# Optimization experiments

Hardware: AMD Instinct MI355X
Metric: run time of the kernel (lower is better)

The kernel has to match this reference:

```python
import jax, jax.numpy as jnp
import numpy as np

NUM_EMBEDDINGS = 8192
EMBEDDING_DIM = 512
COMMITMENT_COST = 0.25


def setup_inputs() -> dict:
    key = jax.random.key(0)
    kx, ke = jax.random.split(key)
    x = jax.random.normal(kx, (32, 512, 512), dtype=jnp.float32)
    # codebook ~ uniform init as in nn.Embedding default-ish; scale is arbitrary for a reference
    codebook = jax.random.normal(ke, (NUM_EMBEDDINGS, EMBEDDING_DIM), dtype=jnp.float32)
    return {"x": x, "codebook": codebook}


def reference(x, codebook):
    # x: [B, T, D], codebook: [K, D]
    input_shape = x.shape
    flat = x.reshape(-1, EMBEDDING_DIM)                     # [N, D]
    x2 = jnp.sum(flat * flat, axis=1, keepdims=True)        # [N, 1]
    e2 = jnp.sum(codebook * codebook, axis=1)               # [K]
    dists = x2 + e2 - 2.0 * jnp.matmul(flat, codebook.T)    # [N, K]
    encoding_indices = jnp.argmin(dists, axis=1)            # [N] int
    min_distances = jnp.min(dists, axis=1)                  # [N]
    quantized = codebook[encoding_indices].reshape(input_shape)  # [B, T, D]
    # straight-through estimator
    quantized_st = x + jax.lax.stop_gradient(quantized - x)
    # losses (sum reduction, matching F.mse_loss(..., reduction='sum'))
    loss_vq = jnp.sum((quantized - jax.lax.stop_gradient(x)) ** 2)
    loss_commit = jnp.sum((x - jax.lax.stop_gradient(quantized)) ** 2)
    # use_ema = False -> loss includes codebook term
    loss = loss_commit * COMMITMENT_COST + loss_vq
    encoding_indices = encoding_indices.reshape(input_shape[:-1])
    min_distances = min_distances.reshape(input_shape[:-1])
    return quantized_st, loss, encoding_indices, min_distances, loss_commit
```

## Files before the change

### kernel.cpp

```cpp
#include <hip/hip_runtime.h>
#include <hip/hip_bf16.h>
#include <math.h>

#define NUM_EMB 8192
#define DIM 512
#define NROWS 16384
#define NPART 4096

typedef unsigned short ushort;
typedef unsigned long long ull;
typedef __attribute__((ext_vector_type(8))) short short8;
typedef __attribute__((ext_vector_type(4))) float floatx4;

__device__ __forceinline__ ushort f2bf(float f) {
    unsigned u = __float_as_uint(f);
    unsigned r = (u + 0x7fffu + ((u >> 16) & 1u)) >> 16;
    return (ushort)r;
}
__device__ __forceinline__ float bf2f(ushort h) {
    return __uint_as_float(((unsigned)h) << 16);
}
__device__ __forceinline__ unsigned fmap(float f) {
    unsigned u = __float_as_uint(f);
    return (u & 0x80000000u) ? ~u : (u | 0x80000000u);
}
__device__ __forceinline__ float funmap(unsigned m) {
    return __uint_as_float((m & 0x80000000u) ? (m ^ 0x80000000u) : ~m);
}
__device__ __forceinline__ void gld16(const void* g, void* l) {
    __builtin_amdgcn_global_load_lds(
        (const __attribute__((address_space(1))) void*)g,
        (__attribute__((address_space(3))) void*)l, 16, 0, 0);
}

__global__ __launch_bounds__(256) void split_rss_k(const float* __restrict__ src,
    ushort* __restrict__ hi, ushort* __restrict__ lo, float* __restrict__ ss,
    ull* __restrict__ packed, int nrows)
{
    int gid  = blockIdx.x * blockDim.x + threadIdx.x;
    int row  = gid >> 6;
    int lane = threadIdx.x & 63;
    if (row >= nrows) return;
    const float4* r = (const float4*)(src + (size_t)row * DIM);
    ushort4* h4 = (ushort4*)(hi + (size_t)row * DIM);
    ushort4* l4 = (ushort4*)(lo + (size_t)row * DIM);
    float s = 0.f;
#pragma unroll
    for (int i = lane; i < DIM / 4; i += 64) {
        float4 v = r[i];
        s += v.x * v.x + v.y * v.y + v.z * v.z + v.w * v.w;
        ushort4 h, l;
        h.x = f2bf(v.x); l.x = f2bf(v.x - bf2f(h.x));
        h.y = f2bf(v.y); l.y = f2bf(v.y - bf2f(h.y));
        h.z = f2bf(v.z); l.z = f2bf(v.z - bf2f(h.z));
        h.w = f2bf(v.w); l.w = f2bf(v.w - bf2f(h.w));
        h4[i] = h; l4[i] = l;
    }
#pragma unroll
    for (int off = 32; off > 0; off >>= 1) s += __shfl_down(s, off, 64);
    if (lane == 0) {
        ss[row] = s;
        if (packed) packed[row] = ~0ull;
    }
}

__global__ __launch_bounds__(512, 2) void dist_mfma_k(
    const ushort* __restrict__ xh, const ushort* __restrict__ xl,
    const ushort* __restrict__ ch, const ushort* __restrict__ cl,
    const float* __restrict__ e2, ull* __restrict__ packed)
{
    __shared__ ushort Ah[2][256 * 32];
    __shared__ ushort Al[2][256 * 32];
    __shared__ ushort Bh[2][256 * 32];
    __shared__ ushort Bl[2][256 * 32];

    const int tid  = threadIdx.x;
    const int lane = tid & 63;
    const int w    = tid >> 6;
    const int wm   = w >> 2, wn = w & 3;
    const int row0 = blockIdx.x * 256;
    const int col0 = blockIdx.y * 256;

    floatx4 acc[8][4];
#pragma unroll
    for (int m = 0; m < 8; ++m)
#pragma unroll
        for (int n = 0; n < 4; ++n) acc[m][n] = (floatx4){0.f, 0.f, 0.f, 0.f};

    const int u = tid & 255, b = tid >> 8;
    const int p = u & 3;
    const int r_h0 = b * 128 + (u >> 2);
    const int r_h1 = r_h0 + 64;
    const int seg0 = (p ^ ((r_h0 >> 1) & 3)) * 8;
    const int seg1 = (p ^ ((r_h1 >> 1) & 3)) * 8;
    const int lo_h0 = (r_h0 * 4 + p) * 8;
    const int lo_h1 = (r_h1 * 4 + p) * 8;
    const int gA0 = (row0 + r_h0) * DIM + seg0;
    const int gA1 = (row0 + r_h1) * DIM + seg1;
    const int gB0 = (col0 + r_h0) * DIM + seg0;
    const int gB1 = (col0 + r_h1) * DIM + seg1;

    const int fr = (lane & 15) * 32 + (((lane >> 4) ^ ((lane >> 1) & 3)) * 8);

    short8 ah[4], al[4], bh[4], bl[4];

#define ISSUE_A(B_, h_, dk_) do { \
    if (h_) { gld16(&xh[gA1 + (dk_)], &Ah[B_][lo_h1]); gld16(&xl[gA1 + (dk_)], &Al[B_][lo_h1]); } \
    else    { gld16(&xh[gA0 + (dk_)], &Ah[B_][lo_h0]); gld16(&xl[gA0 + (dk_)], &Al[B_][lo_h0]); } } while (0)
#define ISSUE_B(B_, h_, dk_) do { \
    if (h_) { gld16(&ch[gB1 + (dk_)], &Bh[B_][lo_h1]); gld16(&cl[gB1 + (dk_)], &Bl[B_][lo_h1]); } \
    else    { gld16(&ch[gB0 + (dk_)], &Bh[B_][lo_h0]); gld16(&cl[gB0 + (dk_)], &Bl[B_][lo_h0]); } } while (0)
#define LOAD_A(B_, mh_) do { \
    _Pragma("unroll") for (int m = 0; m < 4; ++m) { \
        const int o = (wm * 128 + (mh_) * 64 + m * 16) * 32 + fr; \
        ah[m] = *(const short8*)&Ah[B_][o]; \
        al[m] = *(const short8*)&Al[B_][o]; } } while (0)
#define LOAD_B(B_, nh_) do { \
    _Pragma("unroll") for (int n = 0; n < 2; ++n) { \
        const int o = (wn * 64 + (nh_) * 32 + n * 16) * 32 + fr; \
        bh[(nh_) * 2 + n] = *(const short8*)&Bh[B_][o]; \
        bl[(nh_) * 2 + n] = *(const short8*)&Bl[B_][o]; } } while (0)
#define DO_MFMA(mh_, nh_) do { \
    __builtin_amdgcn_s_setprio(1); \
    _Pragma("unroll") for (int m = 0; m < 4; ++m) \
    _Pragma("unroll") for (int n = 0; n < 2; ++n) { \
        acc[(mh_) * 4 + m][(nh_) * 2 + n] = __builtin_amdgcn_mfma_f32_16x16x32_bf16(ah[m], bh[(nh_) * 2 + n], acc[(mh_) * 4 + m][(nh_) * 2 + n], 0, 0, 0); \
        acc[(mh_) * 4 + m][(nh_) * 2 + n] = __builtin_amdgcn_mfma_f32_16x16x32_bf16(ah[m], bl[(nh_) * 2 + n], acc[(mh_) * 4 + m][(nh_) * 2 + n], 0, 0, 0); \
        acc[(mh_) * 4 + m][(nh_) * 2 + n] = __builtin_amdgcn_mfma_f32_16x16x32_bf16(al[m], bh[(nh_) * 2 + n], acc[(mh_) * 4 + m][(nh_) * 2 + n], 0, 0, 0); \
    } \
    __builtin_amdgcn_s_setprio(0); } while (0)

    ISSUE_A(0, 0, 0);
    ISSUE_B(0, 0, 0);
    ISSUE_B(0, 1, 0);
    ISSUE_A(0, 1, 0);
    asm volatile("s_waitcnt vmcnt(0)" ::: "memory");
    __builtin_amdgcn_s_barrier();
    __builtin_amdgcn_sched_barrier(0);

#pragma unroll 1
    for (int t = 0; t < 16; ++t) {
        const int B = t & 1, Bn = B ^ 1;
        const int dkn = (t + 1) * 32;
        const bool pf = (t < 15);

        LOAD_A(B, 0);
        LOAD_B(B, 0);
        if (pf) ISSUE_A(Bn, 0, dkn);
        DO_MFMA(0, 0);
        if (pf) { asm volatile("s_waitcnt vmcnt(4)" ::: "memory"); }
        else    { asm volatile("s_waitcnt vmcnt(2)" ::: "memory"); }
        __builtin_amdgcn_s_barrier();
        __builtin_amdgcn_sched_barrier(0);

        LOAD_B(B, 1);
        if (pf) ISSUE_B(Bn, 0, dkn);
        DO_MFMA(0, 1);
        if (pf) { asm volatile("s_waitcnt vmcnt(4)" ::: "memory"); }
        else    { asm volatile("s_waitcnt vmcnt(0)" ::: "memory"); }
        __builtin_amdgcn_s_barrier();
        __builtin_amdgcn_sched_barrier(0);

        LOAD_A(B, 1);
        if (pf) ISSUE_B(Bn, 1, dkn);
        DO_MFMA(1, 1);
        __builtin_amdgcn_s_barrier();
        __builtin_amdgcn_sched_barrier(0);

        if (pf) ISSUE_A(Bn, 1, dkn);
        DO_MFMA(1, 0);
        if (pf) { asm volatile("s_waitcnt vmcnt(4)" ::: "memory"); }
        __builtin_amdgcn_s_barrier();
        __builtin_amdgcn_sched_barrier(0);
    }

#undef ISSUE_A
#undef ISSUE_B
#undef LOAD_A
#undef LOAD_B
#undef DO_MFMA

    float e2v[4];
    int   cidx[4];
#pragma unroll
    for (int n = 0; n < 4; ++n) {
        cidx[n] = col0 + wn * 64 + n * 16 + (lane & 15);
        e2v[n]  = e2[cidx[n]];
    }
#pragma unroll
    for (int m = 0; m < 8; ++m) {
#pragma unroll
        for (int r = 0; r < 4; ++r) {
            float bv = INFINITY; int bi = 0x7fffffff;
#pragma unroll
            for (int n = 0; n < 4; ++n) {
                float v = e2v[n] - 2.f * acc[m][n][r];
                if (v < bv) { bv = v; bi = cidx[n]; }
            }
#pragma unroll
            for (int mk = 1; mk < 16; mk <<= 1) {
                float ov = __shfl_xor(bv, mk, 64);
                int   oi = __shfl_xor(bi, mk, 64);
                if (ov < bv || (ov == bv && oi < bi)) { bv = ov; bi = oi; }
            }
            if ((lane & 15) == 0) {
                int grow = row0 + wm * 128 + m * 16 + (lane >> 4) * 4 + r;
                ull pack = ((ull)fmap(bv) << 32) | (unsigned)bi;
                atomicMin(&packed[grow], pack);
            }
        }
    }
}

__global__ __launch_bounds__(256) void gather_loss_k(const float* __restrict__ x,
    const float* __restrict__ cb, const ull* __restrict__ packed,
    const float* __restrict__ x2, float* __restrict__ outq,
    float* __restrict__ out_idx, float* __restrict__ out_mind,
    float* __restrict__ partials)
{
    __shared__ float ps[4];
    int gid  = blockIdx.x * blockDim.x + threadIdx.x;
    int row  = gid >> 6;
    int lane = threadIdx.x & 63;
    int w    = threadIdx.x >> 6;
    float s = 0.f;
    if (row < NROWS) {
        ull p = packed[row];
        int k = (int)(p & 0xffffffffull);
        if (lane == 0) {
            out_idx[row]  = (float)k;
            out_mind[row] = x2[row] + funmap((unsigned)(p >> 32));
        }
        const float4* q  = (const float4*)(cb + (size_t)k * DIM);
        const float4* xr = (const float4*)(x + (size_t)row * DIM);
        float4* o = (float4*)(outq + (size_t)row * DIM);
#pragma unroll
        for (int i = lane; i < DIM / 4; i += 64) {
            float4 qv = q[i], xv = xr[i];
            o[i] = qv;
            float dx = xv.x - qv.x, dy = xv.y - qv.y;
            float dz = xv.z - qv.z, dw = xv.w - qv.w;
            s += dx * dx + dy * dy + dz * dz + dw * dw;
        }
    }
#pragma unroll
    for (int off = 32; off > 0; off >>= 1) s += __shfl_down(s, off, 64);
    if (lane == 0) ps[w] = s;
    __syncthreads();
    if (threadIdx.x == 0) partials[blockIdx.x] = ps[0] + ps[1] + ps[2] + ps[3];
}

__global__ __launch_bounds__(256) void finalize_k(const float* __restrict__ partials,
    float* __restrict__ out_loss, float* __restrict__ out_commit)
{
    __shared__ float ps[4];
    int t = threadIdx.x, lane = t & 63, w = t >> 6;
    float s = 0.f;
#pragma unroll
    for (int i = 0; i < NPART / 256; ++i) s += partials[t + 256 * i];
#pragma unroll
    for (int off = 32; off > 0; off >>= 1) s += __shfl_down(s, off, 64);
    if (lane == 0) ps[w] = s;
    __syncthreads();
    if (t == 0) {
        float tot = ps[0] + ps[1] + ps[2] + ps[3];
        *out_loss   = 0.25f * tot + tot;
        *out_commit = tot;
    }
}

#define BM 64
#define BN 64
#define BK 32
#define KSPLIT 4
#define KPER (NUM_EMB / KSPLIT)
#define NCT (KPER / BN)

__global__ __launch_bounds__(256) void rowsumsq_k(const float* __restrict__ a,
                                                  float* __restrict__ out, int nrows)
{
    int gid  = blockIdx.x * blockDim.x + threadIdx.x;
    int row  = gid >> 6;
    int lane = threadIdx.x & 63;
    if (row >= nrows) return;
    const float4* r = (const float4*)(a + (size_t)row * DIM);
    float s = 0.f;
#pragma unroll
    for (int i = lane; i < DIM / 4; i += 64) {
        float4 v = r[i];
        s += v.x * v.x + v.y * v.y + v.z * v.z + v.w * v.w;
    }
#pragma unroll
    for (int off = 32; off > 0; off >>= 1) s += __shfl_down(s, off, 64);
    if (lane == 0) out[row] = s;
}

__global__ __launch_bounds__(256) void dist_argmin_old_k(const float* __restrict__ x,
    const float* __restrict__ cb, const float* __restrict__ e2,
    float* __restrict__ part_m, int* __restrict__ part_i)
{
    __shared__ __align__(16) float As[BK][BM + 4];
    __shared__ __align__(16) float Bs[BK][BN + 4];
    __shared__ float redv[BM][16];
    __shared__ int   redi[BM][16];

    const int row0 = blockIdx.x * BM;
    const int ks   = blockIdx.y;
    const int cbeg = ks * KPER;
    const int t    = threadIdx.x;
    const int tx   = t & 15;
    const int ty   = t >> 4;
    const int ld_d = t & 31;
    const int ld_r = t >> 5;

    float minm[4]; int mini[4];
#pragma unroll
    for (int i = 0; i < 4; ++i) { minm[i] = INFINITY; mini[i] = 0; }

    for (int ct = 0; ct < NCT; ++ct) {
        const int c0 = cbeg + ct * BN;
        float acc[4][4];
#pragma unroll
        for (int i = 0; i < 4; ++i)
#pragma unroll
            for (int j = 0; j < 4; ++j) acc[i][j] = 0.f;
        for (int dc = 0; dc < DIM; dc += BK) {
#pragma unroll
            for (int rr = 0; rr < BM; rr += 8)
                As[ld_d][ld_r + rr] = x[(size_t)(row0 + ld_r + rr) * DIM + dc + ld_d];
#pragma unroll
            for (int rr = 0; rr < BN; rr += 8)
                Bs[ld_d][ld_r + rr] = cb[(size_t)(c0 + ld_r + rr) * DIM + dc + ld_d];
            __syncthreads();
#pragma unroll
            for (int d = 0; d < BK; ++d) {
                float4 av = *(const float4*)&As[d][4 * ty];
                float4 bv = *(const float4*)&Bs[d][4 * tx];
                acc[0][0] += av.x * bv.x; acc[0][1] += av.x * bv.y;
                acc[0][2] += av.x * bv.z; acc[0][3] += av.x * bv.w;
                acc[1][0] += av.y * bv.x; acc[1][1] += av.y * bv.y;
                acc[1][2] += av.y * bv.z; acc[1][3] += av.y * bv.w;
                acc[2][0] += av.z * bv.x; acc[2][1] += av.z * bv.y;
                acc[2][2] += av.z * bv.z; acc[2][3] += av.z * bv.w;
                acc[3][0] += av.w * bv.x; acc[3][1] += av.w * bv.y;
                acc[3][2] += av.w * bv.z; acc[3][3] += av.w * bv.w;
            }
            __syncthreads();
        }
#pragma unroll
        for (int j = 0; j < 4; ++j) {
            const int c = c0 + 4 * tx + j;
            const float e = e2[c];
#pragma unroll
            for (int i = 0; i < 4; ++i) {
                float m = e - 2.f * acc[i][j];
                if (m < minm[i]) { minm[i] = m; mini[i] = c; }
            }
        }
    }
#pragma unroll
    for (int i = 0; i < 4; ++i) {
        redv[4 * ty + i][tx] = minm[i];
        redi[4 * ty + i][tx] = mini[i];
    }
    __syncthreads();
    if (t < BM) {
        float bm = INFINITY; int bi = 0;
#pragma unroll
        for (int c = 0; c < 16; ++c) {
            float v = redv[t][c];
            if (v < bm) { bm = v; bi = redi[t][c]; }
        }
        part_m[(size_t)(row0 + t) * KSPLIT + ks] = bm;
        part_i[(size_t)(row0 + t) * KSPLIT + ks] = bi;
    }
}

__global__ __launch_bounds__(256) void merge_pack_k(const float* __restrict__ part_m,
    const int* __restrict__ part_i, ull* __restrict__ packed)
{
    int row = blockIdx.x * blockDim.x + threadIdx.x;
    if (row >= NROWS) return;
    float bm = INFINITY; int bi = 0;
#pragma unroll
    for (int s = 0; s < KSPLIT; ++s) {
        float v = part_m[(size_t)row * KSPLIT + s];
        if (v < bm) { bm = v; bi = part_i[(size_t)row * KSPLIT + s]; }
    }
    packed[row] = ((ull)fmap(bm) << 32) | (unsigned)bi;
}

extern "C" void kernel_launch(void* const* d_in, const int* in_sizes, int n_in,
                              void* d_out, int out_size, void* d_ws, size_t ws_size,
                              hipStream_t stream)
{
    const float* x  = (const float*)d_in[0];
    const float* cb = (const float*)d_in[1];
    float* out = (float*)d_out;

    float* outq       = out;
    float* out_loss   = out + 8388608;
    float* out_idx    = out + 8388609;
    float* out_mind   = out + 8388609 + 16384;
    float* out_commit = out + 8388609 + 2 * 16384;

    char* ws = (char*)d_ws;
    float* e2      = (float*)ws;   ws += NUM_EMB * 4;
    float* x2      = (float*)ws;   ws += NROWS * 4;
    ull*   packed  = (ull*)ws;     ws += NROWS * 8;
    float* partials= (float*)ws;   ws += NPART * 4;
    ushort* xh = (ushort*)ws;      ws += (size_t)NROWS * DIM * 2;
    ushort* xl = (ushort*)ws;      ws += (size_t)NROWS * DIM * 2;
    ushort* ch = (ushort*)ws;      ws += (size_t)NUM_EMB * DIM * 2;
    ushort* cl = (ushort*)ws;      ws += (size_t)NUM_EMB * DIM * 2;
    size_t need_fast = (size_t)(ws - (char*)d_ws);

    if (ws_size >= need_fast) {
        split_rss_k<<<NROWS / 4, 256, 0, stream>>>(x, xh, xl, x2, packed, NROWS);
        split_rss_k<<<NUM_EMB / 4, 256, 0, stream>>>(cb, ch, cl, e2, (ull*)0, NUM_EMB);
        dim3 grid(NROWS / 256, NUM_EMB / 256);
        dist_mfma_k<<<grid, 512, 0, stream>>>(xh, xl, ch, cl, e2, packed);
    } else {
        rowsumsq_k<<<NUM_EMB / 4, 256, 0, stream>>>(cb, e2, NUM_EMB);
        rowsumsq_k<<<NROWS / 4, 256, 0, stream>>>(x, x2, NROWS);
        float* pm = (float*)((char*)d_ws + NUM_EMB * 4 + NROWS * 4 + NROWS * 8 + NPART * 4);
        int*   pi = (int*)(pm + (size_t)NROWS * KSPLIT);
        dim3 grid(NROWS / BM, KSPLIT);
        dist_argmin_old_k<<<grid, 256, 0, stream>>>(x, cb, e2, pm, pi);
        merge_pack_k<<<NROWS / 256, 256, 0, stream>>>(pm, pi, packed);
    }

    gather_loss_k<<<NROWS / 4, 256, 0, stream>>>(x, cb, packed, x2, outq,
                                                 out_idx, out_mind, partials);
    finalize_k<<<1, 256, 0, stream>>>(partials, out_loss, out_commit);
}
```

Measured before the change: 512.2 us.

## Switch distance GEMM to 32x32x16 MFMA tiles and swizzle block order

Replaces the 16x16x32 bf16 MFMA fragments with 32x32x16 MFMAs, so each wave holds 4x2 floatx16 accumulators and fetches fewer LDS fragments per flop. The fragment addressing, swizzle indices and argmin epilogue are rewritten for the 32-lane row layout, using a 5-step shuffle reduction per row. It also remaps block IDs so consecutively scheduled blocks share codebook column tiles, aiming for better L2 reuse. The epilogue now runs more shuffle steps per row and risks more LDS bank conflicts from the new read pattern.

```diff
diff --git a/kernel.cpp b/kernel.cpp
--- a/kernel.cpp
+++ b/kernel.cpp
@@ -11,6 +11,7 @@
 typedef unsigned long long ull;
 typedef __attribute__((ext_vector_type(8))) short short8;
 typedef __attribute__((ext_vector_type(4))) float floatx4;
+typedef __attribute__((ext_vector_type(16))) float floatx16;
 
 __device__ __forceinline__ ushort f2bf(float f) {
     unsigned u = __float_as_uint(f);
@@ -78,14 +79,19 @@
     const int lane = tid & 63;
     const int w    = tid >> 6;
     const int wm   = w >> 2, wn = w & 3;
-    const int row0 = blockIdx.x * 256;
-    const int col0 = blockIdx.y * 256;
-
-    floatx4 acc[8][4];
-#pragma unroll
-    for (int m = 0; m < 8; ++m)
-#pragma unroll
-        for (int n = 0; n < 4; ++n) acc[m][n] = (floatx4){0.f, 0.f, 0.f, 0.f};
+
+    const int bid  = blockIdx.x + (blockIdx.y << 6);
+    const int sid  = ((bid & 7) << 8) + (bid >> 3);
+    const int row0 = (sid & 63) * 256;
+    const int col0 = (sid >> 6) * 256;
+
+    floatx16 acc[4][2];
+#pragma unroll
+    for (int m = 0; m < 4; ++m)
+#pragma unroll
+        for (int n = 0; n < 2; ++n)
+#pragma unroll
+            for (int r = 0; r < 16; ++r) acc[m][n][r] = 0.f;
 
     const int u = tid & 255, b = tid >> 8;
     const int p = u & 3;
@@ -100,9 +106,11 @@
     const int gB0 = (col0 + r_h0) * DIM + seg0;
     const int gB1 = (col0 + r_h1) * DIM + seg1;
 
-    const int fr = (lane & 15) * 32 + (((lane >> 4) ^ ((lane >> 1) & 3)) * 8);
-
-    short8 ah[4], al[4], bh[4], bl[4];
+    const int lr   = lane & 31;
+    const int fc0  = (((lane >> 5)) ^ ((lane >> 1) & 3)) * 8;
+    const int fc1  = ((2 + (lane >> 5)) ^ ((lane >> 1) & 3)) * 8;
+
+    short8 ah[2][2], al[2][2], bh[2][2], bl[2][2];
 
 #define ISSUE_A(B_, h_, dk_) do { \
     if (h_) { gld16(&xh[gA1 + (dk_)], &Ah[B_][lo_h1]); gld16(&xl[gA1 + (dk_)], &Al[B_][lo_h1]); } \
@@ -111,22 +119,25 @@
     if (h_) { gld16(&ch[gB1 + (dk_)], &Bh[B_][lo_h1]); gld16(&cl[gB1 + (dk_)], &Bl[B_][lo_h1]); } \
     else    { gld16(&ch[gB0 + (dk_)], &Bh[B_][lo_h0]); gld16(&cl[gB0 + (dk_)], &Bl[B_][lo_h0]); } } while (0)
 #define LOAD_A(B_, mh_) do { \
-    _Pragma("unroll") for (int m = 0; m < 4; ++m) { \
-        const int o = (wm * 128 + (mh_) * 64 + m * 16) * 32 + fr; \
-        ah[m] = *(const short8*)&Ah[B_][o]; \
-        al[m] = *(const short8*)&Al[B_][o]; } } while (0)
+    _Pragma("unroll") for (int mm = 0; mm < 2; ++mm) \
+    _Pragma("unroll") for (int s = 0; s < 2; ++s) { \
+        const int o = (wm * 128 + ((mh_) * 2 + mm) * 32 + lr) * 32 + (s ? fc1 : fc0); \
+        ah[mm][s] = *(const short8*)&Ah[B_][o]; \
+        al[mm][s] = *(const short8*)&Al[B_][o]; } } while (0)
 #define LOAD_B(B_, nh_) do { \
-    _Pragma("unroll") for (int n = 0; n < 2; ++n) { \
-        const int o = (wn * 64 + (nh_) * 32 + n * 16) * 32 + fr; \
-        bh[(nh_) * 2 + n] = *(const short8*)&Bh[B_][o]; \
-        bl[(nh_) * 2 + n] = *(const short8*)&Bl[B_][o]; } } while (0)
-#define DO_MFMA(mh_, nh_) do { \
+    _Pragma("unroll") for (int s = 0; s < 2; ++s) { \
+        const int o = (wn * 64 + (nh_) * 32 + lr) * 32 + (s ? fc1 : fc0); \
+        bh[nh_][s] = *(const short8*)&Bh[B_][o]; \
+        bl[nh_][s] = *(const short8*)&Bl[B_][o]; } } while (0)
+#define DO_MFMA(mh_, ni_) do { \
     __builtin_amdgcn_s_setprio(1); \
-    _Pragma("unroll") for (int m = 0; m < 4; ++m) \
-    _Pragma("unroll") for (int n = 0; n < 2; ++n) { \
-        acc[(mh_) * 4 + m][(nh_) * 2 + n] = __builtin_amdgcn_mfma_f32_16x16x32_bf16(ah[m], bh[(nh_) * 2 + n], acc[(mh_) * 4 + m][(nh_) * 2 + n], 0, 0, 0); \
-        acc[(mh_) * 4 + m][(nh_) * 2 + n] = __builtin_amdgcn_mfma_f32_16x16x32_bf16(ah[m], bl[(nh_) * 2 + n], acc[(mh_) * 4 + m][(nh_) * 2 + n], 0, 0, 0); \
-        acc[(mh_) * 4 + m][(nh_) * 2 + n] = __builtin_amdgcn_mfma_f32_16x16x32_bf16(al[m], bh[(nh_) * 2 + n], acc[(mh_) * 4 + m][(nh_) * 2 + n], 0, 0, 0); \
+    _Pragma("unroll") for (int s = 0; s < 2; ++s) { \
+        _Pragma("unroll") for (int mm = 0; mm < 2; ++mm) \
+            acc[(mh_) * 2 + mm][ni_] = __builtin_amdgcn_mfma_f32_32x32x16_bf16(ah[mm][s], bh[ni_][s], acc[(mh_) * 2 + mm][ni_], 0, 0, 0); \
+        _Pragma("unroll") for (int mm = 0; mm < 2; ++mm) \
+            acc[(mh_) * 2 + mm][ni_] = __builtin_amdgcn_mfma_f32_32x32x16_bf16(ah[mm][s], bl[ni_][s], acc[(mh_) * 2 + mm][ni_], 0, 0, 0); \
+        _Pragma("unroll") for (int mm = 0; mm < 2; ++mm) \
+            acc[(mh_) * 2 + mm][ni_] = __builtin_amdgcn_mfma_f32_32x32x16_bf16(al[mm][s], bh[ni_][s], acc[(mh_) * 2 + mm][ni_], 0, 0, 0); \
     } \
     __builtin_amdgcn_s_setprio(0); } while (0)
 
@@ -180,31 +191,30 @@
 #undef LOAD_B
 #undef DO_MFMA
 
-    float e2v[4];
-    int   cidx[4];
-#pragma unroll
-    for (int n = 0; n < 4; ++n) {
-        cidx[n] = col0 + wn * 64 + n * 16 + (lane & 15);
-        e2v[n]  = e2[cidx[n]];
-    }
-#pragma unroll
-    for (int m = 0; m < 8; ++m) {
-#pragma unroll
-        for (int r = 0; r < 4; ++r) {
-            float bv = INFINITY; int bi = 0x7fffffff;
-#pragma unroll
-            for (int n = 0; n < 4; ++n) {
-                float v = e2v[n] - 2.f * acc[m][n][r];
-                if (v < bv) { bv = v; bi = cidx[n]; }
-            }
-#pragma unroll
-            for (int mk = 1; mk < 16; mk <<= 1) {
+    float e2v[2];
+    int   cidx[2];
+    cidx[0] = col0 + wn * 64 + lr;
+    cidx[1] = cidx[0] + 32;
+    e2v[0]  = e2[cidx[0]];
+    e2v[1]  = e2[cidx[1]];
+    const int rbase = row0 + wm * 128 + ((lane >> 5) << 2);
+#pragma unroll
+    for (int mi = 0; mi < 4; ++mi) {
+#pragma unroll
+        for (int rg = 0; rg < 16; ++rg) {
+            float v0 = e2v[0] - 2.f * acc[mi][0][rg];
+            float v1 = e2v[1] - 2.f * acc[mi][1][rg];
+            float bv; int bi;
+            if (v1 < v0) { bv = v1; bi = cidx[1]; }
+            else         { bv = v0; bi = cidx[0]; }
+#pragma unroll
+            for (int mk = 1; mk < 32; mk <<= 1) {
                 float ov = __shfl_xor(bv, mk, 64);
                 int   oi = __shfl_xor(bi, mk, 64);
                 if (ov < bv || (ov == bv && oi < bi)) { bv = ov; bi = oi; }
             }
-            if ((lane & 15) == 0) {
-                int grow = row0 + wm * 128 + m * 16 + (lane >> 4) * 4 + r;
+            if ((lane & 31) == 0) {
+                int grow = rbase + mi * 32 + (rg & 3) + ((rg >> 2) << 3);
                 ull pack = ((ull)fmap(bv) << 32) | (unsigned)bi;
                 atomicMin(&packed[grow], pack);
             }
```

Result: slower. 683.7 us (+33.5%).
